# Kernel tuning notes

Measured on AMD Instinct MI355X. Metric: run time of the kernel, lower is better.

## Reference

```python
import jax, jax.numpy as jnp
import numpy as np

N, E, H, G, L = 50000, 640000, 128, 8, 3

def setup_inputs() -> dict:
    key = jax.random.key(0)
    ks = jax.random.split(key, 10)
    s = 1.0 / np.sqrt(H)
    return {
        "x": jax.random.normal(ks[0], (N, H), jnp.float32),
        "query": jax.random.normal(ks[1], (G, H), jnp.float32),
        "Wl": jax.random.normal(ks[2], (L, H, H), jnp.float32) * s,
        "bl": jax.random.normal(ks[3], (L, H), jnp.float32) * s,
        "Wr": jax.random.normal(ks[4], (L, H, H), jnp.float32) * s,
        "Wlin": jax.random.normal(ks[5], (H, H), jnp.float32) * s,
        "blin": jax.random.normal(ks[6], (H,), jnp.float32) * s,
        "edge_index": jax.random.randint(ks[7], (2, E), 0, N, jnp.int64),
        "batch_vec": jnp.sort(jax.random.randint(ks[8], (N,), 0, G, jnp.int64)),
    }

def reference(x, query, Wl, bl, Wr, Wlin, blin, edge_index, batch_vec):
    src, dst = edge_index[0], edge_index[1]
    n = x.shape[0]
    for i in range(L):
        # SAGEConv(aggr='max'): gather neighbor feats, scatter-max to dst
        m = jax.ops.segment_max(x[src], dst, num_segments=n)  # [N,H]
        m = jnp.where(jnp.isfinite(m), m, 0.0)  # isolated nodes -> 0 (PyG)
        x = jax.nn.relu(m @ Wl[i].T + bl[i] + x @ Wr[i].T)
    x = x @ Wlin.T + blin  # encoder final linear
    # cosine scoring per graph, vectorized via batch_vec
    xn = x / jnp.linalg.norm(x, axis=1, keepdims=True).clip(1e-12)
    qn = query / jnp.linalg.norm(query, axis=1, keepdims=True).clip(1e-12)
    scores = jnp.sum(xn * qn[batch_vec], axis=1)  # [N]
    return scores
```

## Files before the change

### kernel.cpp

```cpp
#include <hip/hip_runtime.h>
#include <math.h>

#define H 128

typedef _Float16 half8 __attribute__((ext_vector_type(8)));
typedef float f32x16 __attribute__((ext_vector_type(16)));
typedef int int4v __attribute__((ext_vector_type(4)));

__device__ __forceinline__ half8 h8max(half8 a, half8 b) {
#if defined(__has_builtin) && __has_builtin(__builtin_elementwise_max)
    return __builtin_elementwise_max(a, b);
#else
    half8 r;
#pragma unroll
    for (int j = 0; j < 8; ++j) r[j] = a[j] > b[j] ? a[j] : b[j];
    return r;
#endif
}

__device__ __forceinline__ half8 h8shfl_xor(half8 v, int mask) {
    int4v iv;
    __builtin_memcpy(&iv, &v, 16);
#pragma unroll
    for (int j = 0; j < 4; ++j) iv[j] = __shfl_xor(iv[j], mask, 64);
    half8 r;
    __builtin_memcpy(&r, &iv, 16);
    return r;
}


__global__ __launch_bounds__(256) void scan_atomic(const int* __restrict__ deg,
                                                   int* __restrict__ offsets,
                                                   int* __restrict__ gcur, int N) {
    __shared__ int buf[256];
    __shared__ int sbase;
    int tid = threadIdx.x;
    int i = blockIdx.x * 256 + tid;
    int v = (i < N) ? deg[i] : 0;
    int incl = v;
    buf[tid] = v;
    __syncthreads();
#pragma unroll
    for (int off = 1; off < 256; off <<= 1) {
        int t = (tid >= off) ? buf[tid - off] : 0;
        __syncthreads();
        incl += t;
        buf[tid] = incl;
        __syncthreads();
    }
    if (tid == 255) sbase = atomicAdd(gcur, incl);
    __syncthreads();
    if (i < N) offsets[i] = sbase + incl - v;
}

__global__ __launch_bounds__(256) void fill_adj(const int* __restrict__ ei, int E,
                                                const int* __restrict__ offsets,
                                                int* __restrict__ cursor,
                                                int* __restrict__ adj,
                                                int* __restrict__ adjp32) {
    int e = blockIdx.x * 256 + threadIdx.x;
    if (e < E) {
        int s = ei[e];
        int d = ei[E + e];
        int pos = atomicAdd(&cursor[d], 1);
        adj[offsets[d] + pos] = s;
        if (pos < 32) adjp32[(size_t)d * 32 + pos] = s;
    }
}


__global__ __launch_bounds__(256) void prep_all(
    const int* __restrict__ ei, int E, int* __restrict__ deg,
    const float* __restrict__ x, const float* __restrict__ query,
    const float* __restrict__ Wl, const float* __restrict__ Wr,
    const float* __restrict__ Wlin, _Float16* __restrict__ xh,
    _Float16* __restrict__ wimg, float* __restrict__ qn, int n8, int HB, int SB,
    int WB) {
    int b = blockIdx.x;
    int tid = threadIdx.x;
    if (b < HB) {
        int e = b * 256 + tid;
        if (e < E) atomicAdd(&deg[ei[E + e]], 1);
    } else if (b < HB + SB) {
        int i = (b - HB) * 256 + tid;
        if (i < n8) {
            const float4* x4 = (const float4*)x;
            float4 u = x4[(size_t)i * 2], v = x4[(size_t)i * 2 + 1];
            float f[8] = {u.x, u.y, u.z, u.w, v.x, v.y, v.z, v.w};
            half8 h;
#pragma unroll
            for (int j = 0; j < 8; ++j) h[j] = (_Float16)f[j];
            *(half8*)(xh + (size_t)i * 8) = h;
        }
    } else if (b < HB + SB + WB) {
        int gidx = (b - HB - SB) * 256 + tid;
        if (gidx < 7 * 2048) {
            int mat = gidx / 2048;
            int rem = gidx - mat * 2048;
            int kc4 = rem >> 9;
            int r2 = rem & 511;
            int s = r2 >> 6;
            int lane = r2 & 63;
            int ks = s >> 2;
            int colgrp = s & 3;
            int lhi = lane >> 5, l31 = lane & 31;
            int n = colgrp * 32 + l31;
            int g16 = kc4 * 4 + ks * 2 + lhi;
            const float* src = (mat == 6) ? Wlin
                             : ((mat & 1) ? Wr + (mat >> 1) * H * H
                                          : Wl + (mat >> 1) * H * H);
            const float* p = src + n * H + g16 * 8;
            half8 h, l;
#pragma unroll
            for (int j = 0; j < 8; ++j) {
                float v = p[j];
                _Float16 hh = (_Float16)v;
                h[j] = hh;
                l[j] = (_Float16)(v - (float)hh);
            }
            size_t base = (size_t)mat * 32768 + (size_t)kc4 * 8192 +
                          (size_t)s * 1024 + (size_t)lane * 16;
            *(half8*)(wimg + base) = h;
            *(half8*)(wimg + base + 8) = l;
        }
    } else {
        int g = b - HB - SB - WB;
        __shared__ float part[4];
        float v = (tid < 128) ? query[g * H + tid] : 0.f;
        float ss = v * v;
#pragma unroll
        for (int off = 32; off > 0; off >>= 1) ss += __shfl_xor(ss, off, 64);
        if ((tid & 63) == 0) part[tid >> 6] = ss;
        __syncthreads();
        float tot = part[0] + part[1];
        if (tid < 128) qn[g * H + tid] = v / fmaxf(sqrtf(tot), 1e-12f);
    }
}


template <bool FINAL>
__global__ __launch_bounds__(256, 6) void layer_fused(
    const half8* __restrict__ Xh, const int* __restrict__ deg,
    const int* __restrict__ offsets, const int* __restrict__ adj,
    const int* __restrict__ adjp32, const _Float16* __restrict__ Bimg,
    const float* __restrict__ bias, _Float16* __restrict__ Yh,
    const _Float16* __restrict__ BimgF, const float* __restrict__ blin,
    const float* __restrict__ qn, const int* __restrict__ bv,
    float* __restrict__ out, int N) {
    __shared__ __align__(16) _Float16 sU[4096];
    __shared__ __align__(16) _Float16 sX[4096];

    int tid = threadIdx.x;
    int w = tid >> 6;
    int lane = tid & 63;
    int l31 = lane & 31;
    int lhi = lane >> 5;
    int n0 = blockIdx.x * 32;

    const half8 hz = {(_Float16)0.f, (_Float16)0.f, (_Float16)0.f, (_Float16)0.f,
                      (_Float16)0.f, (_Float16)0.f, (_Float16)0.f, (_Float16)0.f};

    {
#pragma unroll
        for (int t = 0; t < 2; ++t) {
            int idx = tid + t * 256;
            int row = idx >> 4;
            int g = idx & 15;
            int nn = n0 + row;
            half8 h = hz;
            if (nn < N) h = Xh[(size_t)nn * 16 + g];
            *(half8*)&sX[row * 128 + ((g ^ (row & 15)) << 3)] = h;
        }
    }

    {
        int sub = lane >> 4;
        int lf = lane & 15;
        const _Float16 ni = (_Float16)(-INFINITY);
        const half8 ninf = {ni, ni, ni, ni, ni, ni, ni, ni};
        int nd8 = n0 + w * 8;
        int nn = nd8 + (lane & 7);
        int degv = (nn < N) ? deg[nn] : 0;

        int dmx = degv;
#pragma unroll
        for (int off = 1; off <= 4; off <<= 1) {
            int t = __shfl_xor(dmx, off, 64);
            dmx = t > dmx ? t : dmx;
        }

        if (dmx <= 32) {
            int c0 = nd8 + (lane >> 4);
            c0 = c0 < N ? c0 : N - 1;
            int c1 = nd8 + 4 + (lane >> 4);
            c1 = c1 < N ? c1 : N - 1;
            int r0 = adjp32[(size_t)c0 * 32 + (lane & 15)];
            int r1 = adjp32[(size_t)c1 * 32 + (lane & 15)];
            int r2 = adjp32[(size_t)c0 * 32 + 16 + (lane & 15)];
            int r3 = adjp32[(size_t)c1 * 32 + 16 + (lane & 15)];
#pragma unroll
            for (int i = 0; i < 8; ++i) {
                int d = __shfl(degv, i, 64);
                int base = (i & 3) << 4;
                int j0 = sub, j1 = 4 + sub, j2 = 8 + sub, j3 = 12 + sub;
                int i0 = __shfl(i < 4 ? r0 : r1, base | (j0 < d ? j0 : 0), 64);
                int i1 = __shfl(i < 4 ? r0 : r1, base | (j1 < d ? j1 : 0), 64);
                int i2 = __shfl(i < 4 ? r0 : r1, base | (j2 < d ? j2 : 0), 64);
                int i3 = __shfl(i < 4 ? r0 : r1, base | (j3 < d ? j3 : 0), 64);
                half8 v0 = Xh[(size_t)i0 * 16 + lf];
                half8 v1 = Xh[(size_t)i1 * 16 + lf];
                half8 v2 = Xh[(size_t)i2 * 16 + lf];
                half8 v3 = Xh[(size_t)i3 * 16 + lf];
                half8 acc = h8max(h8max(v0, v1), h8max(v2, v3));
                if (d > 16) {
                    int k4 = (16 + sub) < d ? sub : 0;
                    int k5 = (20 + sub) < d ? 4 + sub : 0;
                    int k6 = (24 + sub) < d ? 8 + sub : 0;
                    int k7 = (28 + sub) < d ? 12 + sub : 0;
                    int i4 = __shfl(i < 4 ? r2 : r3, base | k4, 64);
                    int i5 = __shfl(i < 4 ? r2 : r3, base | k5, 64);
                    int i6 = __shfl(i < 4 ? r2 : r3, base | k6, 64);
                    int i7 = __shfl(i < 4 ? r2 : r3, base | k7, 64);
                    half8 u0 = Xh[(size_t)i4 * 16 + lf];
                    half8 u1 = Xh[(size_t)i5 * 16 + lf];
                    half8 u2 = Xh[(size_t)i6 * 16 + lf];
                    half8 u3 = Xh[(size_t)i7 * 16 + lf];
                    acc = h8max(acc, h8max(h8max(u0, u1), h8max(u2, u3)));
                }
                acc = h8max(acc, h8shfl_xor(acc, 16));
                acc = h8max(acc, h8shfl_xor(acc, 32));
                if (d == 0) acc = hz;
                int row = w * 8 + i;
                if (sub == 0) *(half8*)&sU[row * 128 + ((lf ^ (row & 15)) << 3)] = acc;
            }
        } else {
            int ndc = nn < N ? nn : N - 1;
            int e0v = offsets[ndc];
            for (int i = 0; i < 8; ++i) {
                int e0 = __shfl(e0v, i, 64);
                int d = __shfl(degv, i, 64);
                int row = w * 8 + i;
                half8 acc = ninf;
                for (int base = 0; base < d; base += 16) {
                    half8 v[4];
#pragma unroll
                    for (int q = 0; q < 4; ++q) {
                        int j = base + q * 4 + sub;
                        int idx = adj[e0 + (j < d ? j : d - 1)];
                        v[q] = Xh[(size_t)idx * 16 + lf];
                    }
                    acc = h8max(acc, h8max(h8max(v[0], v[1]), h8max(v[2], v[3])));
                }
                acc = h8max(acc, h8shfl_xor(acc, 16));
                acc = h8max(acc, h8shfl_xor(acc, 32));
                if (d == 0) acc = hz;
                if (sub == 0) *(half8*)&sU[row * 128 + ((lf ^ (row & 15)) << 3)] = acc;
            }
        }
    }
    __syncthreads();

    f32x16 acc;
    {
        float bvv = bias[w * 32 + l31];
#pragma unroll
        for (int r = 0; r < 16; ++r) acc[r] = bvv;
    }

    int rl = l31;
    int col = w * 32 + l31;

#pragma unroll
    for (int kc4 = 0; kc4 < 4; ++kc4) {
#pragma unroll
        for (int ks = 0; ks < 2; ++ks) {
            int g16 = kc4 * 4 + ks * 2 + lhi;
            int posA = g16 ^ (rl & 15);
            half8 ah = *(const half8*)&sU[rl * 128 + posA * 8];
            size_t boff =
                (size_t)kc4 * 8192 + (size_t)(ks * 4 + w) * 1024 + (size_t)lane * 16;
            half8 bh = *(const half8*)&Bimg[boff];
            half8 bl2 = *(const half8*)&Bimg[boff + 8];
            acc = __builtin_amdgcn_mfma_f32_32x32x16_f16(ah, bh, acc, 0, 0, 0);
            acc = __builtin_amdgcn_mfma_f32_32x32x16_f16(ah, bl2, acc, 0, 0, 0);
        }
    }

    const _Float16* Br = Bimg + 32768;
#pragma unroll
    for (int kc4 = 0; kc4 < 4; ++kc4) {
#pragma unroll
        for (int ks = 0; ks < 2; ++ks) {
            int g16 = kc4 * 4 + ks * 2 + lhi;
            int posA = g16 ^ (rl & 15);
            half8 ah = *(const half8*)&sX[rl * 128 + posA * 8];
            size_t boff =
                (size_t)kc4 * 8192 + (size_t)(ks * 4 + w) * 1024 + (size_t)lane * 16;
            half8 bh = *(const half8*)&Br[boff];
            half8 bl2 = *(const half8*)&Br[boff + 8];
            acc = __builtin_amdgcn_mfma_f32_32x32x16_f16(ah, bh, acc, 0, 0, 0);
            acc = __builtin_amdgcn_mfma_f32_32x32x16_f16(ah, bl2, acc, 0, 0, 0);
        }
    }

    if constexpr (!FINAL) {
#pragma unroll
        for (int r = 0; r < 16; ++r) {
            int row = n0 + (r & 3) + 8 * (r >> 2) + 4 * lhi;
            if (row < N) Yh[(size_t)row * H + col] = (_Float16)fmaxf(acc[r], 0.f);
        }
    } else {
        __syncthreads();
#pragma unroll
        for (int r = 0; r < 16; ++r) {
            int rloc = (r & 3) + 8 * (r >> 2) + 4 * lhi;
            sU[rloc * 128 + (((col >> 3) ^ (rloc & 15)) << 3) + (col & 7)] =
                (_Float16)fmaxf(acc[r], 0.f);
        }
        f32x16 acc2;
        {
            float b = blin[col];
#pragma unroll
            for (int r = 0; r < 16; ++r) acc2[r] = b;
        }
        int arow = n0 + l31;
        arow = arow < N ? arow : N - 1;
        int gl = bv[arow];
        __syncthreads();

#pragma unroll
        for (int kc4 = 0; kc4 < 4; ++kc4) {
#pragma unroll
            for (int ks = 0; ks < 2; ++ks) {
                int g16 = kc4 * 4 + ks * 2 + lhi;
                int posA = g16 ^ (rl & 15);
                half8 ah = *(const half8*)&sU[rl * 128 + posA * 8];
                size_t boff = (size_t)kc4 * 8192 + (size_t)(ks * 4 + w) * 1024 +
                              (size_t)lane * 16;
                half8 bh = *(const half8*)&BimgF[boff];
                half8 bl2 = *(const half8*)&BimgF[boff + 8];
                acc2 = __builtin_amdgcn_mfma_f32_32x32x16_f16(ah, bh, acc2, 0, 0, 0);
                acc2 = __builtin_amdgcn_mfma_f32_32x32x16_f16(ah, bl2, acc2, 0, 0, 0);
            }
        }

        float* sP = (float*)sX;
#pragma unroll
        for (int r = 0; r < 16; ++r) {
            int rloc = (r & 3) + 8 * (r >> 2) + 4 * lhi;
            int g = __shfl(gl, rloc, 32);
            float y = acc2[r];
            float q = qn[(size_t)g * H + col];
            float ss = y * y;
            float sd = y * q;
#pragma unroll
            for (int off = 1; off <= 16; off <<= 1) {
                ss += __shfl_xor(ss, off, 64);
                sd += __shfl_xor(sd, off, 64);
            }
            if (l31 == 0) {
                sP[(rloc * 4 + w) * 2] = ss;
                sP[(rloc * 4 + w) * 2 + 1] = sd;
            }
        }
        __syncthreads();
        if (tid < 32) {
            int row = n0 + tid;
            if (row < N) {
                float ss = 0.f, sd = 0.f;
#pragma unroll
                for (int q = 0; q < 4; ++q) {
                    ss += sP[(tid * 4 + q) * 2];
                    sd += sP[(tid * 4 + q) * 2 + 1];
                }
                out[row] = sd / fmaxf(sqrtf(ss), 1e-12f);
            }
        }
    }
}


extern "C" void kernel_launch(void* const* d_in, const int* in_sizes, int n_in,
                              void* d_out, int out_size, void* d_ws, size_t ws_size,
                              hipStream_t stream) {
    const float* x = (const float*)d_in[0];
    const float* query = (const float*)d_in[1];
    const float* Wl = (const float*)d_in[2];
    const float* bl = (const float*)d_in[3];
    const float* Wr = (const float*)d_in[4];
    const float* Wlin = (const float*)d_in[5];
    const float* blin = (const float*)d_in[6];
    const int* ei = (const int*)d_in[7];
    const int* bv = (const int*)d_in[8];
    float* out = (float*)d_out;

    const int N = in_sizes[0] / H;
    const int E = in_sizes[7] / 2;
    const int G = in_sizes[1] / H;

    char* p = (char*)d_ws;
    auto alloc = [&](size_t bytes) {
        char* r = p;
        p += (bytes + 255) & ~(size_t)255;
        return r;
    };
    int* deg = (int*)alloc((size_t)(2 * N + 1) * sizeof(int));
    int* cursor = deg + N;
    int* gcur = deg + 2 * N;
    int* offsets = (int*)alloc((size_t)N * sizeof(int));
    int* adj = (int*)alloc((size_t)E * sizeof(int));
    int* adjp32 = (int*)alloc((size_t)N * 32 * sizeof(int));
    float* qn = (float*)alloc((size_t)G * H * sizeof(float));
    _Float16* wimg = (_Float16*)alloc((size_t)7 * 32768 * sizeof(_Float16));
    size_t actH = (size_t)N * H * sizeof(_Float16);
    _Float16* xah = (_Float16*)alloc(actH);
    _Float16* xbh = (_Float16*)alloc(actH);

    hipMemsetAsync(deg, 0, (size_t)(2 * N + 1) * sizeof(int), stream);
    hipMemsetAsync(adjp32, 0, (size_t)N * 32 * sizeof(int), stream);

    const int n8 = N * H / 8;
    const int HB = (E + 255) / 256;
    const int SB = (n8 + 255) / 256;
    const int WB = (7 * 2048 + 255) / 256;
    prep_all<<<HB + SB + WB + G, 256, 0, stream>>>(ei, E, deg, x, query, Wl, Wr,
                                                   Wlin, xah, wimg, qn, n8, HB,
                                                   SB, WB);
    scan_atomic<<<(N + 255) / 256, 256, 0, stream>>>(deg, offsets, gcur, N);
    fill_adj<<<(E + 255) / 256, 256, 0, stream>>>(ei, E, offsets, cursor, adj,
                                                  adjp32);

    const int NGm = (N + 31) / 32;

    layer_fused<false><<<NGm, 256, 0, stream>>>(
        (const half8*)xah, deg, offsets, adj, adjp32, wimg + (size_t)0 * 65536,
        bl + 0 * H, xbh, nullptr, nullptr, nullptr, nullptr, nullptr, N);
    layer_fused<false><<<NGm, 256, 0, stream>>>(
        (const half8*)xbh, deg, offsets, adj, adjp32, wimg + (size_t)1 * 65536,
        bl + 1 * H, xah, nullptr, nullptr, nullptr, nullptr, nullptr, N);
    layer_fused<true><<<NGm, 256, 0, stream>>>(
        (const half8*)xah, deg, offsets, adj, adjp32, wimg + (size_t)2 * 65536,
        bl + 2 * H, nullptr, wimg + (size_t)6 * 32768, blin, qn, bv, out, N);
}
```

Baseline: 283.3 us.

## Double block width, split layer GEMM across wave halves, unfuse final projection

The layer kernel now uses 512 threads per 32-node block, so each wave gathers neighbor maxima for 4 nodes instead of 8. The two GEMMs (aggregated times Wl and self times Wr) run on separate wave halves, and their partial sums are combined through shared memory. The final linear plus cosine scoring moves out of the last layer into a separate kernel, which adds a launch and an extra fp16 activation round trip through global memory. The aim is more gather parallelism and shorter per-wave GEMM chains, at the cost of extra syncs and a cross-wave reduction.

```diff
diff --git a/kernel.cpp b/kernel.cpp
--- a/kernel.cpp
+++ b/kernel.cpp
@@ -138,20 +138,21 @@
 }
 
 
-template <bool FINAL>
-__global__ __launch_bounds__(256, 6) void layer_fused(
+template <bool FINAL_UNUSED>
+__global__ __launch_bounds__(512, 8) void layer_fused(
     const half8* __restrict__ Xh, const int* __restrict__ deg,
     const int* __restrict__ offsets, const int* __restrict__ adj,
     const int* __restrict__ adjp32, const _Float16* __restrict__ Bimg,
-    const float* __restrict__ bias, _Float16* __restrict__ Yh,
-    const _Float16* __restrict__ BimgF, const float* __restrict__ blin,
-    const float* __restrict__ qn, const int* __restrict__ bv,
-    float* __restrict__ out, int N) {
-    __shared__ __align__(16) _Float16 sU[4096];
-    __shared__ __align__(16) _Float16 sX[4096];
+    const float* __restrict__ bias, _Float16* __restrict__ Yh, int N) {
+    __shared__ __align__(16) unsigned char smem[16384];
+    _Float16* sU = (_Float16*)smem;
+    _Float16* sX = (_Float16*)(smem + 8192);
+    float* comb = (float*)smem;
 
     int tid = threadIdx.x;
     int w = tid >> 6;
+    int wq = w & 3;
+    int wh = w >> 2;
     int lane = tid & 63;
     int l31 = lane & 31;
     int lhi = lane >> 5;
@@ -161,16 +162,12 @@
                       (_Float16)0.f, (_Float16)0.f, (_Float16)0.f, (_Float16)0.f};
 
     {
-#pragma unroll
-        for (int t = 0; t < 2; ++t) {
-            int idx = tid + t * 256;
-            int row = idx >> 4;
-            int g = idx & 15;
-            int nn = n0 + row;
-            half8 h = hz;
-            if (nn < N) h = Xh[(size_t)nn * 16 + g];
-            *(half8*)&sX[row * 128 + ((g ^ (row & 15)) << 3)] = h;
-        }
+        int row = tid >> 4;
+        int g = tid & 15;
+        int nn = n0 + row;
+        half8 h = hz;
+        if (nn < N) h = Xh[(size_t)nn * 16 + g];
+        *(half8*)&sX[row * 128 + ((g ^ (row & 15)) << 3)] = h;
     }
 
     {
@@ -178,35 +175,32 @@
         int lf = lane & 15;
         const _Float16 ni = (_Float16)(-INFINITY);
         const half8 ninf = {ni, ni, ni, ni, ni, ni, ni, ni};
-        int nd8 = n0 + w * 8;
-        int nn = nd8 + (lane & 7);
-        int degv = (nn < N) ? deg[nn] : 0;
+        int nd4 = n0 + w * 4;
+        int node = nd4 + sub;
+        int nodec = node < N ? node : N - 1;
+        int degv = (node < N) ? deg[node] : 0;
 
         int dmx = degv;
-#pragma unroll
-        for (int off = 1; off <= 4; off <<= 1) {
-            int t = __shfl_xor(dmx, off, 64);
+        {
+            int t = __shfl_xor(dmx, 16, 64);
             dmx = t > dmx ? t : dmx;
+            t = __shfl_xor(dmx, 32, 64);
+            dmx = t > dmx ? t : dmx;
         }
 
         if (dmx <= 32) {
-            int c0 = nd8 + (lane >> 4);
-            c0 = c0 < N ? c0 : N - 1;
-            int c1 = nd8 + 4 + (lane >> 4);
-            c1 = c1 < N ? c1 : N - 1;
-            int r0 = adjp32[(size_t)c0 * 32 + (lane & 15)];
-            int r1 = adjp32[(size_t)c1 * 32 + (lane & 15)];
-            int r2 = adjp32[(size_t)c0 * 32 + 16 + (lane & 15)];
-            int r3 = adjp32[(size_t)c1 * 32 + 16 + (lane & 15)];
-#pragma unroll
-            for (int i = 0; i < 8; ++i) {
-                int d = __shfl(degv, i, 64);
-                int base = (i & 3) << 4;
+            int r0 = adjp32[(size_t)nodec * 32 + lf];
+            int r1 = 0;
+            if (dmx > 16) r1 = adjp32[(size_t)nodec * 32 + 16 + lf];
+#pragma unroll
+            for (int i = 0; i < 4; ++i) {
+                int d = __shfl(degv, i << 4, 64);
+                int base = i << 4;
                 int j0 = sub, j1 = 4 + sub, j2 = 8 + sub, j3 = 12 + sub;
-                int i0 = __shfl(i < 4 ? r0 : r1, base | (j0 < d ? j0 : 0), 64);
-                int i1 = __shfl(i < 4 ? r0 : r1, base | (j1 < d ? j1 : 0), 64);
-                int i2 = __shfl(i < 4 ? r0 : r1, base | (j2 < d ? j2 : 0), 64);
-                int i3 = __shfl(i < 4 ? r0 : r1, base | (j3 < d ? j3 : 0), 64);
+                int i0 = __shfl(r0, base | (j0 < d ? j0 : 0), 64);
+                int i1 = __shfl(r0, base | (j1 < d ? j1 : 0), 64);
+                int i2 = __shfl(r0, base | (j2 < d ? j2 : 0), 64);
+                int i3 = __shfl(r0, base | (j3 < d ? j3 : 0), 64);
                 half8 v0 = Xh[(size_t)i0 * 16 + lf];
                 half8 v1 = Xh[(size_t)i1 * 16 + lf];
                 half8 v2 = Xh[(size_t)i2 * 16 + lf];
@@ -217,10 +211,10 @@
                     int k5 = (20 + sub) < d ? 4 + sub : 0;
                     int k6 = (24 + sub) < d ? 8 + sub : 0;
                     int k7 = (28 + sub) < d ? 12 + sub : 0;
-                    int i4 = __shfl(i < 4 ? r2 : r3, base | k4, 64);
-                    int i5 = __shfl(i < 4 ? r2 : r3, base | k5, 64);
-                    int i6 = __shfl(i < 4 ? r2 : r3, base | k6, 64);
-                    int i7 = __shfl(i < 4 ? r2 : r3, base | k7, 64);
+                    int i4 = __shfl(r1, base | k4, 64);
+                    int i5 = __shfl(r1, base | k5, 64);
+                    int i6 = __shfl(r1, base | k6, 64);
+                    int i7 = __shfl(r1, base | k7, 64);
                     half8 u0 = Xh[(size_t)i4 * 16 + lf];
                     half8 u1 = Xh[(size_t)i5 * 16 + lf];
                     half8 u2 = Xh[(size_t)i6 * 16 + lf];
@@ -230,16 +224,15 @@
                 acc = h8max(acc, h8shfl_xor(acc, 16));
                 acc = h8max(acc, h8shfl_xor(acc, 32));
                 if (d == 0) acc = hz;
-                int row = w * 8 + i;
+                int row = w * 4 + i;
                 if (sub == 0) *(half8*)&sU[row * 128 + ((lf ^ (row & 15)) << 3)] = acc;
             }
         } else {
-            int ndc = nn < N ? nn : N - 1;
-            int e0v = offsets[ndc];
-            for (int i = 0; i < 8; ++i) {
-                int e0 = __shfl(e0v, i, 64);
-                int d = __shfl(degv, i, 64);
-                int row = w * 8 + i;
+            int e0v = offsets[nodec];
+            for (int i = 0; i < 4; ++i) {
+                int e0 = __shfl(e0v, i << 4, 64);
+                int d = __shfl(degv, i << 4, 64);
+                int row = w * 4 + i;
                 half8 acc = ninf;
                 for (int base = 0; base < d; base += 16) {
                     half8 v[4];
@@ -261,14 +254,16 @@
     __syncthreads();
 
     f32x16 acc;
+    int col = wq * 32 + l31;
     {
-        float bvv = bias[w * 32 + l31];
-#pragma unroll
-        for (int r = 0; r < 16; ++r) acc[r] = bvv;
+        float b0 = (wh == 0) ? bias[col] : 0.f;
+#pragma unroll
+        for (int r = 0; r < 16; ++r) acc[r] = b0;
     }
 
     int rl = l31;
-    int col = w * 32 + l31;
+    const _Float16* A = wh ? sX : sU;
+    const _Float16* B = Bimg + (size_t)wh * 32768;
 
 #pragma unroll
     for (int kc4 = 0; kc4 < 4; ++kc4) {
@@ -276,7 +271,88 @@
         for (int ks = 0; ks < 2; ++ks) {
             int g16 = kc4 * 4 + ks * 2 + lhi;
             int posA = g16 ^ (rl & 15);
-            half8 ah = *(const half8*)&sU[rl * 128 + posA * 8];
+            half8 ah = *(const half8*)&A[rl * 128 + posA * 8];
+            size_t boff =
+                (size_t)kc4 * 8192 + (size_t)(ks * 4 + wq) * 1024 + (size_t)lane * 16;
+            half8 bh = *(const half8*)&B[boff];
+            half8 bl2 = *(const half8*)&B[boff + 8];
+            acc = __builtin_amdgcn_mfma_f32_32x32x16_f16(ah, bh, acc, 0, 0, 0);
+            acc = __builtin_amdgcn_mfma_f32_32x32x16_f16(ah, bl2, acc, 0, 0, 0);
+        }
+    }
+
+    __syncthreads();
+
+    if (wh == 1) {
+#pragma unroll
+        for (int r = 0; r < 16; ++r) {
+            int rloc = (r & 3) + 8 * (r >> 2) + 4 * lhi;
+            comb[wq * 1024 + rloc * 32 + l31] = acc[r];
+        }
+    }
+    __syncthreads();
+
+    if (wh == 0) {
+#pragma unroll
+        for (int r = 0; r < 16; ++r) {
+            int rloc = (r & 3) + 8 * (r >> 2) + 4 * lhi;
+            float y = acc[r] + comb[wq * 1024 + rloc * 32 + l31];
+            int row = n0 + rloc;
+            if (row < N) Yh[(size_t)row * H + col] = (_Float16)fmaxf(y, 0.f);
+        }
+    }
+}
+
+
+__global__ __launch_bounds__(256) void final_mfma6(
+    const half8* __restrict__ Xh, const _Float16* __restrict__ Bimg,
+    const float* __restrict__ blin, const float* __restrict__ qn,
+    const int* __restrict__ bv, float* __restrict__ out, int N) {
+    __shared__ __align__(16) _Float16 sA[4096];
+
+    int tid = threadIdx.x;
+    int w = tid >> 6;
+    int lane = tid & 63;
+    int l31 = lane & 31;
+    int lhi = lane >> 5;
+    int n0 = blockIdx.x * 32;
+
+    {
+        const half8 hz = {(_Float16)0.f, (_Float16)0.f, (_Float16)0.f, (_Float16)0.f,
+                          (_Float16)0.f, (_Float16)0.f, (_Float16)0.f, (_Float16)0.f};
+#pragma unroll
+        for (int t = 0; t < 2; ++t) {
+            int idx = tid + t * 256;
+            int row = idx >> 4;
+            int g = idx & 15;
+            int nn = n0 + row;
+            half8 h = hz;
+            if (nn < N) h = Xh[(size_t)nn * 16 + g];
+            *(half8*)&sA[row * 128 + ((g ^ (row & 15)) << 3)] = h;
+        }
+    }
+
+    int arow = n0 + l31;
+    arow = arow < N ? arow : N - 1;
+    int gl = bv[arow];
+
+    f32x16 acc;
+    int col = w * 32 + l31;
+    {
+        float b = blin[col];
+#pragma unroll
+        for (int r = 0; r < 16; ++r) acc[r] = b;
+    }
+    int rl = l31;
+    __syncthreads();
+
+#pragma unroll
+    for (int kc4 = 0; kc4 < 4; ++kc4) {
+#pragma unroll
+        for (int ks = 0; ks < 2; ++ks) {
+            int g16 = kc4 * 4 + ks * 2 + lhi;
+            int posA = g16 ^ (rl & 15);
+            half8 ah = *(const half8*)&sA[rl * 128 + posA * 8];
             size_t boff =
                 (size_t)kc4 * 8192 + (size_t)(ks * 4 + w) * 1024 + (size_t)lane * 16;
             half8 bh = *(const half8*)&Bimg[boff];
@@ -286,95 +362,37 @@
         }
     }
 
-    const _Float16* Br = Bimg + 32768;
-#pragma unroll
-    for (int kc4 = 0; kc4 < 4; ++kc4) {
-#pragma unroll
-        for (int ks = 0; ks < 2; ++ks) {
-            int g16 = kc4 * 4 + ks * 2 + lhi;
-            int posA = g16 ^ (rl & 15);
-            half8 ah = *(const half8*)&sX[rl * 128 + posA * 8];
-            size_t boff =
-                (size_t)kc4 * 8192 + (size_t)(ks * 4 + w) * 1024 + (size_t)lane * 16;
-            half8 bh = *(const half8*)&Br[boff];
-            half8 bl2 = *(const half8*)&Br[boff + 8];
-            acc = __builtin_amdgcn_mfma_f32_32x32x16_f16(ah, bh, acc, 0, 0, 0);
-            acc = __builtin_amdgcn_mfma_f32_32x32x16_f16(ah, bl2, acc, 0, 0, 0);
-        }
-    }
-
-    if constexpr (!FINAL) {
-#pragma unroll
-        for (int r = 0; r < 16; ++r) {
-            int row = n0 + (r & 3) + 8 * (r >> 2) + 4 * lhi;
-            if (row < N) Yh[(size_t)row * H + col] = (_Float16)fmaxf(acc[r], 0.f);
-        }
-    } else {
-        __syncthreads();
-#pragma unroll
-        for (int r = 0; r < 16; ++r) {
-            int rloc = (r & 3) + 8 * (r >> 2) + 4 * lhi;
-            sU[rloc * 128 + (((col >> 3) ^ (rloc & 15)) << 3) + (col & 7)] =
-                (_Float16)fmaxf(acc[r], 0.f);
-        }
-        f32x16 acc2;
-        {
-            float b = blin[col];
-#pragma unroll
-            for (int r = 0; r < 16; ++r) acc2[r] = b;
-        }
-        int arow = n0 + l31;
-        arow = arow < N ? arow : N - 1;
-        int gl = bv[arow];
-        __syncthreads();
-
-#pragma unroll
-        for (int kc4 = 0; kc4 < 4; ++kc4) {
-#pragma unroll
-            for (int ks = 0; ks < 2; ++ks) {
-                int g16 = kc4 * 4 + ks * 2 + lhi;
-                int posA = g16 ^ (rl & 15);
-                half8 ah = *(const half8*)&sU[rl * 128 + posA * 8];
-                size_t boff = (size_t)kc4 * 8192 + (size_t)(ks * 4 + w) * 1024 +
-                              (size_t)lane * 16;
-                half8 bh = *(const half8*)&BimgF[boff];
-                half8 bl2 = *(const half8*)&BimgF[boff + 8];
-                acc2 = __builtin_amdgcn_mfma_f32_32x32x16_f16(ah, bh, acc2, 0, 0, 0);
-                acc2 = __builtin_amdgcn_mfma_f32_32x32x16_f16(ah, bl2, acc2, 0, 0, 0);
+    __syncthreads();
+    float* sP = (float*)sA;
+#pragma unroll
+    for (int r = 0; r < 16; ++r) {
+        int rloc = (r & 3) + 8 * (r >> 2) + 4 * lhi;
+        int g = __shfl(gl, rloc, 32);
+        float y = acc[r];
+        float q = qn[(size_t)g * H + col];
+        float ss = y * y;
+        float sd = y * q;
+#pragma unroll
+        for (int off = 1; off <= 16; off <<= 1) {
+            ss += __shfl_xor(ss, off, 64);
+            sd += __shfl_xor(sd, off, 64);
+        }
+        if (l31 == 0) {
+            sP[(rloc * 4 + w) * 2] = ss;
+            sP[(rloc * 4 + w) * 2 + 1] = sd;
+        }
+    }
+    __syncthreads();
+    if (tid < 32) {
+        int row = n0 + tid;
+        if (row < N) {
+            float ss = 0.f, sd = 0.f;
+#pragma unroll
+            for (int q = 0; q < 4; ++q) {
+                ss += sP[(tid * 4 + q) * 2];
+                sd += sP[(tid * 4 + q) * 2 + 1];
             }
-        }
-
-        float* sP = (float*)sX;
-#pragma unroll
-        for (int r = 0; r < 16; ++r) {
-            int rloc = (r & 3) + 8 * (r >> 2) + 4 * lhi;
-            int g = __shfl(gl, rloc, 32);
-            float y = acc2[r];
-            float q = qn[(size_t)g * H + col];
-            float ss = y * y;
-            float sd = y * q;
-#pragma unroll
-            for (int off = 1; off <= 16; off <<= 1) {
-                ss += __shfl_xor(ss, off, 64);
-                sd += __shfl_xor(sd, off, 64);
-            }
-            if (l31 == 0) {
-                sP[(rloc * 4 + w) * 2] = ss;
-                sP[(rloc * 4 + w) * 2 + 1] = sd;
-            }
-        }
-        __syncthreads();
-        if (tid < 32) {
-            int row = n0 + tid;
-            if (row < N) {
-                float ss = 0.f, sd = 0.f;
-#pragma unroll
-                for (int q = 0; q < 4; ++q) {
-                    ss += sP[(tid * 4 + q) * 2];
-                    sd += sP[(tid * 4 + q) * 2 + 1];
-                }
-                out[row] = sd / fmaxf(sqrtf(ss), 1e-12f);
-            }
+            out[row] = sd / fmaxf(sqrtf(ss), 1e-12f);
         }
     }
 }
@@ -432,13 +450,15 @@
 
     const int NGm = (N + 31) / 32;
 
-    layer_fused<false><<<NGm, 256, 0, stream>>>(
+    layer_fused<false><<<NGm, 512, 0, stream>>>(
         (const half8*)xah, deg, offsets, adj, adjp32, wimg + (size_t)0 * 65536,
-        bl + 0 * H, xbh, nullptr, nullptr, nullptr, nullptr, nullptr, N);
-    layer_fused<false><<<NGm, 256, 0, stream>>>(
+        bl + 0 * H, xbh, N);
+    layer_fused<false><<<NGm, 512, 0, stream>>>(
         (const half8*)xbh, deg, offsets, adj, adjp32, wimg + (size_t)1 * 65536,
-        bl + 1 * H, xah, nullptr, nullptr, nullptr, nullptr, nullptr, N);
-    layer_fused<true><<<NGm, 256, 0, stream>>>(
+        bl + 1 * H, xah, N);
+    layer_fused<false><<<NGm, 512, 0, stream>>>(
         (const half8*)xah, deg, offsets, adj, adjp32, wimg + (size_t)2 * 65536,
-        bl + 2 * H, nullptr, wimg + (size_t)6 * 32768, blin, qn, bv, out, N);
-}
+        bl + 2 * H, xbh, N);
+    final_mfma6<<<NGm, 256, 0, stream>>>(
+        (const half8*)xbh, wimg + (size_t)6 * 32768, blin, qn, bv, out, N);
+}
```

Measured after the change: 289.7 us. 1.02x slower.
